# Kernel tuning notes

Hardware: AMD Instinct MI355X
Metric: run time of the kernel (lower is better)

## Reference

```python
import jax, jax.numpy as jnp
import numpy as np

B, LQ, LM, D, H = 2, 2048, 2048, 1024, 16
DH = D // H  # 64

def setup_inputs() -> dict:
    key = jax.random.key(0)
    ks = jax.random.split(key, 11)
    s = 0.02
    return {
        "query": jax.random.normal(ks[0], (B, LQ, D), jnp.float32),
        "memory": jax.random.normal(ks[1], (B, LM, D), jnp.float32),
        "memory_bias": jax.random.normal(ks[2], (B, LM), jnp.float32),
        "Wq": jax.random.normal(ks[3], (D, D), jnp.float32) * s,
        "bq": jnp.zeros((D,), jnp.float32),
        "Wk": jax.random.normal(ks[4], (D, D), jnp.float32) * s,
        "bk": jnp.zeros((D,), jnp.float32),
        "Wv": jax.random.normal(ks[5], (D, D), jnp.float32) * s,
        "bv": jnp.zeros((D,), jnp.float32),
        "Wo": jax.random.normal(ks[6], (D, D), jnp.float32) * s,
        "bo": jnp.zeros((D,), jnp.float32),
    }

def reference(query, memory, memory_bias, Wq, bq, Wk, bk, Wv, bv, Wo, bo):
    # QKV projections, split into heads: [B, L, H, DH]
    q = (query @ Wq + bq).reshape(B, LQ, H, DH)
    k = (memory @ Wk + bk).reshape(B, LM, H, DH)
    v = (memory @ Wv + bv).reshape(B, LM, H, DH)
    q = q * (DH ** -0.5)
    # logits: [B, H, Lq, Lk] (matches torch.einsum('btnh,bfnh->bnft', k, q))
    logits = jnp.einsum("bfnh,btnh->bnft", q, k)
    logits = logits + memory_bias[:, None, None, :]  # bias [B, Lm] -> [B,1,1,Lk]
    weights = jax.nn.softmax(logits, axis=-1)
    # dropout omitted (eval / rate 0 for correctness baseline)
    attn = jnp.einsum("bnft,btnh->bfnh", weights, v).reshape(B, LQ, D)
    return attn @ Wo + bo  # [B, Lq, output_depth]
```

## Files before the change

kernel.cpp:

```cpp
#include <hip/hip_runtime.h>
#include <hip/hip_bf16.h>
#include <math.h>


typedef __bf16 bf16;
typedef __bf16 bf16x4 __attribute__((ext_vector_type(4)));
typedef __bf16 bf16x8 __attribute__((ext_vector_type(8)));
typedef float f32x4 __attribute__((ext_vector_type(4)));

#define MFMA16(a, b, c) __builtin_amdgcn_mfma_f32_16x16x32_bf16((a), (b), (c), 0, 0, 0)

__device__ inline float exp2_hw(float x) {
    float r; asm("v_exp_f32 %0, %1" : "=v"(r) : "v"(x)); return r;
}

__device__ inline void gload_lds16(const bf16* g, bf16* l) {
    __builtin_amdgcn_global_load_lds(
        (const __attribute__((address_space(1))) void*)g,
        (__attribute__((address_space(3))) void*)l, 16, 0, 0);
}

__global__ __launch_bounds__(256) void cvt_kernel(
    const float* __restrict__ X0, const float* __restrict__ X1,
    bf16* __restrict__ Y0, bf16* __restrict__ Y1)
{
    const float* X = blockIdx.y ? X1 : X0;
    bf16* Y = blockIdx.y ? Y1 : Y0;
    const size_t i = ((size_t)blockIdx.x * 256 + threadIdx.x) * 8;
    float4 f0 = *(const float4*)&X[i];
    float4 f1 = *(const float4*)&X[i + 4];
    bf16x8 h;
    h[0] = (bf16)f0.x; h[1] = (bf16)f0.y; h[2] = (bf16)f0.z; h[3] = (bf16)f0.w;
    h[4] = (bf16)f1.x; h[5] = (bf16)f1.y; h[6] = (bf16)f1.z; h[7] = (bf16)f1.w;
    *(bf16x8*)&Y[i] = h;
}

__global__ __launch_bounds__(256) void transpose_cvt_kernel(
    const float* __restrict__ W0, const float* __restrict__ W1,
    const float* __restrict__ W2, const float* __restrict__ W3,
    bf16* __restrict__ T0, bf16* __restrict__ T1,
    bf16* __restrict__ T2, bf16* __restrict__ T3)
{
    __shared__ float Ls[64][65];
    const float* W; bf16* T;
    switch (blockIdx.z) {
        case 0:  W = W0; T = T0; break;
        case 1:  W = W1; T = T1; break;
        case 2:  W = W2; T = T2; break;
        default: W = W3; T = T3; break;
    }
    const int t = threadIdx.x;
    const int n0 = blockIdx.x * 64, k0 = blockIdx.y * 64;
    const int g = t >> 4, c = (t & 15) * 4;

    #pragma unroll
    for (int p = 0; p < 4; ++p) {
        const int row = p * 16 + g;
        float4 f = *(const float4*)&W[(size_t)(k0 + row) * 1024 + n0 + c];
        Ls[row][c + 0] = f.x; Ls[row][c + 1] = f.y;
        Ls[row][c + 2] = f.z; Ls[row][c + 3] = f.w;
    }
    __syncthreads();
    #pragma unroll
    for (int p = 0; p < 4; ++p) {
        const int n = p * 16 + g;
        bf16x4 h;
        h[0] = (bf16)Ls[c + 0][n]; h[1] = (bf16)Ls[c + 1][n];
        h[2] = (bf16)Ls[c + 2][n]; h[3] = (bf16)Ls[c + 3][n];
        *(bf16x4*)&T[(size_t)(n0 + n) * 1024 + k0 + c] = h;
    }
}

template <typename TO>
__global__ __launch_bounds__(256) void gemm_kernel(
    const bf16* __restrict__ A, const bf16* __restrict__ WT,
    const float* __restrict__ bias, TO* __restrict__ out,
    float alpha, int mode)
{
    __shared__ __align__(16) bf16 As[2][128 * 64];
    __shared__ __align__(16) bf16 Bs[2][64 * 64];

    const int fid = blockIdx.x + (blockIdx.y << 4);
    const int swz = (fid & 7) * 64 + (fid >> 3);
    const int n0 = (swz & 15) * 64;
    const int m0 = (swz >> 4) * 128;

    const int tid = threadIdx.x;
    const int w = tid >> 6, lane = tid & 63;
    const int lr = lane & 15, lg = lane >> 4;
    const int wm = (w >> 1) * 64, wn = (w & 1) * 32;

    const int arow0 = w * 32 + (lane >> 3);
    const int brow0 = w * 16 + (lane >> 3);
    const int sch = lane & 7;

    f32x4 acc[4][2] = {};

    auto stageG = [&](int kt, int bi) {
        #pragma unroll
        for (int p = 0; p < 4; ++p) {
            const int row = arow0 + p * 8;
            const int xc = ((sch ^ (row & 7)) << 3);
            gload_lds16(&A[(size_t)(m0 + row) * 1024 + kt + xc],
                        &As[bi][row * 64 + sch * 8]);
        }
        #pragma unroll
        for (int p = 0; p < 2; ++p) {
            const int row = brow0 + p * 8;
            const int xc = ((sch ^ (row & 7)) << 3);
            gload_lds16(&WT[(size_t)(n0 + row) * 1024 + kt + xc],
                        &Bs[bi][row * 64 + sch * 8]);
        }
    };

    stageG(0, 0);
    __syncthreads();

    int cur = 0;
    #pragma unroll 1
    for (int t = 0; t < 16; ++t) {
        if (t < 15) stageG((t + 1) * 64, cur ^ 1);

        #pragma unroll
        for (int ks = 0; ks < 2; ++ks) {
            const int c = (((ks * 4 + lg) ^ (lr & 7)) << 3);
            bf16x8 af[4], bfv[2];
            #pragma unroll
            for (int mt = 0; mt < 4; ++mt)
                af[mt] = *(const bf16x8*)&As[cur][(wm + mt * 16 + lr) * 64 + c];
            #pragma unroll
            for (int nt = 0; nt < 2; ++nt)
                bfv[nt] = *(const bf16x8*)&Bs[cur][(wn + nt * 16 + lr) * 64 + c];
            #pragma unroll
            for (int nt = 0; nt < 2; ++nt)
                #pragma unroll
                for (int mt = 0; mt < 4; ++mt)
                    acc[mt][nt] = MFMA16(af[mt], bfv[nt], acc[mt][nt]);
        }
        __syncthreads();
        cur ^= 1;
    }

    #pragma unroll
    for (int nt = 0; nt < 2; ++nt) {
        const int n = n0 + wn + nt * 16 + lr;
        const float bv = bias[n];
        #pragma unroll
        for (int mt = 0; mt < 4; ++mt) {
            #pragma unroll
            for (int i = 0; i < 4; ++i) {
                const int m = m0 + wm + mt * 16 + lg * 4 + i;
                const float v = (acc[mt][nt][i] + bv) * alpha;
                if (mode == 0) {
                    out[(size_t)m * 1024 + n] = (TO)v;
                } else {
                    const int b = m >> 11, t2 = m & 2047;
                    out[((size_t)(b << 10) + n) * 2048 + t2] = (TO)v;
                }
            }
        }
    }
}

__global__ __launch_bounds__(512, 4) void attn_kernel(
    const bf16* __restrict__ Q, const bf16* __restrict__ K,
    const bf16* __restrict__ Vt, const float* __restrict__ mbias,
    bf16* __restrict__ Oout)
{
    __shared__ __align__(16) bf16 Kbuf[2][4096];
    __shared__ __align__(16) bf16 Vbuf[2][4096];
    __shared__ bf16 Ps[8][16][76];

    const int tid = threadIdx.x;
    const int w = tid >> 6, lane = tid & 63;
    const int lr = lane & 15, lg = lane >> 4;

    const int fid = blockIdx.x + (blockIdx.y << 4) + (blockIdx.z << 8);
    const int swz = (fid & 7) * 64 + (fid >> 3);
    const int qt = swz & 15, h = (swz >> 4) & 15, b = swz >> 8;
    const int qrow = qt * 128 + w * 16;

    const size_t qo = (size_t)(b * 2048 + qrow + lr) * 1024 + h * 64;
    bf16x8 qf[2];
    qf[0] = *(const bf16x8*)&Q[qo + lg * 8];
    qf[1] = *(const bf16x8*)&Q[qo + 32 + lg * 8];

    const bf16* Kb = K + (size_t)b * 2048 * 1024 + h * 64;
    const bf16* Vb = Vt + ((size_t)b * 1024 + h * 64) * 2048;
    const float* bp = mbias + b * 2048 + lr;

    float m_run[4];
    f32x4 of[4] = {};
    f32x4 ofl = {};
    #pragma unroll
    for (int i = 0; i < 4; ++i) m_run[i] = -INFINITY;

    bf16x8 ones8;
    #pragma unroll
    for (int j = 0; j < 8; ++j) ones8[j] = (bf16)1.0f;

    const int chunk = w * 64 + lane;
    const int sR = chunk >> 3, scs = (chunk & 7) ^ (sR & 7);
    auto stage = [&](int t, int bi) {
        gload_lds16(Kb + (size_t)(t * 64 + sR) * 1024 + scs * 8,
                    &Kbuf[bi][chunk * 8]);
        gload_lds16(Vb + (size_t)sR * 2048 + t * 64 + scs * 8,
                    &Vbuf[bi][chunk * 8]);
    };

    stage(0, 0);
    float bvv[4];
    #pragma unroll
    for (int nt = 0; nt < 4; ++nt) bvv[nt] = bp[nt * 16] * 1.44269504f;

    #pragma unroll 1
    for (int it = 0; it < 32; ++it) {
        const int cur = it & 1;
        stage(it < 31 ? it + 1 : 31, cur ^ 1);
        asm volatile("s_waitcnt vmcnt(2)" ::: "memory");
        __builtin_amdgcn_s_barrier();
        __builtin_amdgcn_sched_barrier(0);

        f32x4 s[4];
        #pragma unroll
        for (int nt = 0; nt < 4; ++nt) {
            s[nt][0] = bvv[nt]; s[nt][1] = bvv[nt];
            s[nt][2] = bvv[nt]; s[nt][3] = bvv[nt];
        }
        #pragma unroll
        for (int ks = 0; ks < 2; ++ks) {
            const int cw = (((ks * 4 + lg) ^ (lr & 7)) << 3);
            bf16x8 kf[4];
            #pragma unroll
            for (int nt = 0; nt < 4; ++nt)
                kf[nt] = *(const bf16x8*)&Kbuf[cur][(nt * 16 + lr) * 64 + cw];
            __builtin_amdgcn_s_setprio(1);
            #pragma unroll
            for (int nt = 0; nt < 4; ++nt)
                s[nt] = MFMA16(qf[ks], kf[nt], s[nt]);
            __builtin_amdgcn_s_setprio(0);
        }

        float rml[4];
        #pragma unroll
        for (int i = 0; i < 4; ++i)
            rml[i] = fmaxf(fmaxf(s[0][i], s[1][i]), fmaxf(s[2][i], s[3][i]));
        bool need = false;
        #pragma unroll
        for (int i = 0; i < 4; ++i)
            need = need || (rml[i] > m_run[i] + 8.f);

        if (__any(need)) {
            #pragma unroll
            for (int off = 1; off < 16; off <<= 1)
                #pragma unroll
                for (int i = 0; i < 4; ++i)
                    rml[i] = fmaxf(rml[i], __shfl_xor(rml[i], off, 64));
            #pragma unroll
            for (int i = 0; i < 4; ++i) {
                const float mnew = fmaxf(m_run[i], rml[i]);
                const float al = exp2_hw(m_run[i] - mnew);
                m_run[i] = mnew;
                ofl[i] *= al;
                #pragma unroll
                for (int dt = 0; dt < 4; ++dt) of[dt][i] *= al;
            }
        }

        bp += (it < 31) ? 64 : 0;
        #pragma unroll
        for (int nt = 0; nt < 4; ++nt) bvv[nt] = bp[nt * 16] * 1.44269504f;

        #pragma unroll
        for (int nt = 0; nt < 4; ++nt)
            #pragma unroll
            for (int i = 0; i < 4; ++i) {
                const float p = exp2_hw(s[nt][i] - m_run[i]);
                Ps[w][lg * 4 + i][nt * 16 + lr] = (bf16)p;
            }

        bf16x8 vf[2][4];
        #pragma unroll
        for (int ks = 0; ks < 2; ++ks) {
            const int cw = (((ks * 4 + lg) ^ (lr & 7)) << 3);
            #pragma unroll
            for (int dt = 0; dt < 4; ++dt)
                vf[ks][dt] = *(const bf16x8*)&Vbuf[cur][(dt * 16 + lr) * 64 + cw];
        }
        bf16x8 pa0 = *(const bf16x8*)&Ps[w][lr][lg * 8];
        bf16x8 pa1 = *(const bf16x8*)&Ps[w][lr][32 + lg * 8];
        __builtin_amdgcn_s_setprio(1);
        #pragma unroll
        for (int dt = 0; dt < 4; ++dt) of[dt] = MFMA16(pa0, vf[0][dt], of[dt]);
        ofl = MFMA16(pa0, ones8, ofl);
        #pragma unroll
        for (int dt = 0; dt < 4; ++dt) of[dt] = MFMA16(pa1, vf[1][dt], of[dt]);
        ofl = MFMA16(pa1, ones8, ofl);
        __builtin_amdgcn_s_setprio(0);

        __builtin_amdgcn_sched_barrier(0);
        __builtin_amdgcn_s_barrier();
    }

    const size_t ob = (size_t)(b * 2048 + qrow + lg * 4) * 1024 + h * 64;
    #pragma unroll
    for (int i = 0; i < 4; ++i) {
        const float inv = 1.0f / ofl[i];
        #pragma unroll
        for (int dt = 0; dt < 4; ++dt)
            Oout[ob + (size_t)i * 1024 + dt * 16 + lr] = (bf16)(of[dt][i] * inv);
    }
}

extern "C" void kernel_launch(void* const* d_in, const int* in_sizes, int n_in,
                              void* d_out, int out_size, void* d_ws, size_t ws_size,
                              hipStream_t stream) {
    const float* query  = (const float*)d_in[0];
    const float* memory = (const float*)d_in[1];
    const float* mbias  = (const float*)d_in[2];
    const float* Wq = (const float*)d_in[3];
    const float* bq = (const float*)d_in[4];
    const float* Wk = (const float*)d_in[5];
    const float* bk = (const float*)d_in[6];
    const float* Wv = (const float*)d_in[7];
    const float* bv = (const float*)d_in[8];
    const float* Wo = (const float*)d_in[9];
    const float* bo = (const float*)d_in[10];
    float* out = (float*)d_out;

    const size_t SZ = 4096ull * 1024ull * sizeof(bf16);
    const size_t WZ = 1024ull * 1024ull * sizeof(bf16);
    char* ws = (char*)d_ws;
    bf16* Qp  = (bf16*)(ws);
    bf16* Kp  = (bf16*)(ws + SZ);
    bf16* Vtp = (bf16*)(ws + 2 * SZ);
    bf16* Ap  = (bf16*)(ws + 3 * SZ);
    bf16* WTq = (bf16*)(ws + 4 * SZ);
    bf16* WTk = (bf16*)(ws + 4 * SZ + WZ);
    bf16* WTv = (bf16*)(ws + 4 * SZ + 2 * WZ);
    bf16* WTo = (bf16*)(ws + 4 * SZ + 3 * WZ);

    dim3 blk(256);
    cvt_kernel<<<dim3(2048, 2), blk, 0, stream>>>(query, memory, Kp, Ap);
    transpose_cvt_kernel<<<dim3(16, 16, 4), blk, 0, stream>>>(
        Wq, Wk, Wv, Wo, WTq, WTk, WTv, WTo);

    dim3 gg(16, 32);
    gemm_kernel<bf16><<<gg, blk, 0, stream>>>(Kp, WTq, bq, Qp,  0.18033688f, 0);
    gemm_kernel<bf16><<<gg, blk, 0, stream>>>(Ap, WTk, bk, Kp,  1.0f, 0);
    gemm_kernel<bf16><<<gg, blk, 0, stream>>>(Ap, WTv, bv, Vtp, 1.0f, 1);
    attn_kernel<<<dim3(16, 16, 2), dim3(512), 0, stream>>>(Qp, Kp, Vtp, mbias, Ap);
    gemm_kernel<float><<<gg, blk, 0, stream>>>(Ap, WTo, bo, out, 1.0f, 0);
}
```

Measured before the change: 150.1 us.

## Fuse K/V projections and rework attention into transposed register-resident softmax

Replaces the separate K and V projection GEMMs with one kernel that reads each activation tile once and computes both outputs. The attention kernel computes S transposed (K as the A operand), so P stays in registers as the B operand of the PV MFMA. This removes the shared-memory P staging and the per-row max shuffles. It also deepens the K/V pipeline to four slots with prefetch distance two, permutes K rows to match the register P layout, and vectorizes the bias loads and output stores. The costs are more LDS per block (which may lower occupancy), more registers from the doubled accumulators in the fused GEMM, and a riskier row permutation.

```diff
diff --git a/kernel.cpp b/kernel.cpp
--- a/kernel.cpp
+++ b/kernel.cpp
@@ -162,14 +162,107 @@
     }
 }
 
+__global__ __launch_bounds__(256) void gemm_kv_kernel(
+    const bf16* __restrict__ A, const bf16* __restrict__ WTk,
+    const bf16* __restrict__ WTv, const float* __restrict__ bk,
+    const float* __restrict__ bv, bf16* __restrict__ Kout,
+    bf16* __restrict__ Vtout)
+{
+    __shared__ __align__(16) bf16 As[2][128 * 64];
+    __shared__ __align__(16) bf16 Bk[2][64 * 64];
+    __shared__ __align__(16) bf16 Bv[2][64 * 64];
+
+    const int fid = blockIdx.x + (blockIdx.y << 4);
+    const int swz = (fid & 7) * 64 + (fid >> 3);
+    const int n0 = (swz & 15) * 64;
+    const int m0 = (swz >> 4) * 128;
+
+    const int tid = threadIdx.x;
+    const int w = tid >> 6, lane = tid & 63;
+    const int lr = lane & 15, lg = lane >> 4;
+    const int wm = (w >> 1) * 64, wn = (w & 1) * 32;
+
+    const int arow0 = w * 32 + (lane >> 3);
+    const int brow0 = w * 16 + (lane >> 3);
+    const int sch = lane & 7;
+
+    f32x4 accK[4][2] = {}, accV[4][2] = {};
+
+    auto stageG = [&](int kt, int bi) {
+        #pragma unroll
+        for (int p = 0; p < 4; ++p) {
+            const int row = arow0 + p * 8;
+            const int xc = ((sch ^ (row & 7)) << 3);
+            gload_lds16(&A[(size_t)(m0 + row) * 1024 + kt + xc],
+                        &As[bi][row * 64 + sch * 8]);
+        }
+        #pragma unroll
+        for (int p = 0; p < 2; ++p) {
+            const int row = brow0 + p * 8;
+            const int xc = ((sch ^ (row & 7)) << 3);
+            gload_lds16(&WTk[(size_t)(n0 + row) * 1024 + kt + xc],
+                        &Bk[bi][row * 64 + sch * 8]);
+            gload_lds16(&WTv[(size_t)(n0 + row) * 1024 + kt + xc],
+                        &Bv[bi][row * 64 + sch * 8]);
+        }
+    };
+
+    stageG(0, 0);
+    __syncthreads();
+
+    int cur = 0;
+    #pragma unroll 1
+    for (int t = 0; t < 16; ++t) {
+        if (t < 15) stageG((t + 1) * 64, cur ^ 1);
+
+        #pragma unroll
+        for (int ks = 0; ks < 2; ++ks) {
+            const int c = (((ks * 4 + lg) ^ (lr & 7)) << 3);
+            bf16x8 af[4], bkf[2], bvf[2];
+            #pragma unroll
+            for (int mt = 0; mt < 4; ++mt)
+                af[mt] = *(const bf16x8*)&As[cur][(wm + mt * 16 + lr) * 64 + c];
+            #pragma unroll
+            for (int nt = 0; nt < 2; ++nt) {
+                bkf[nt] = *(const bf16x8*)&Bk[cur][(wn + nt * 16 + lr) * 64 + c];
+                bvf[nt] = *(const bf16x8*)&Bv[cur][(wn + nt * 16 + lr) * 64 + c];
+            }
+            #pragma unroll
+            for (int nt = 0; nt < 2; ++nt)
+                #pragma unroll
+                for (int mt = 0; mt < 4; ++mt) {
+                    accK[mt][nt] = MFMA16(af[mt], bkf[nt], accK[mt][nt]);
+                    accV[mt][nt] = MFMA16(af[mt], bvf[nt], accV[mt][nt]);
+                }
+        }
+        __syncthreads();
+        cur ^= 1;
+    }
+
+    #pragma unroll
+    for (int nt = 0; nt < 2; ++nt) {
+        const int n = n0 + wn + nt * 16 + lr;
+        const float bkv = bk[n], bvv = bv[n];
+        #pragma unroll
+        for (int mt = 0; mt < 4; ++mt) {
+            #pragma unroll
+            for (int i = 0; i < 4; ++i) {
+                const int m = m0 + wm + mt * 16 + lg * 4 + i;
+                Kout[(size_t)m * 1024 + n] = (bf16)(accK[mt][nt][i] + bkv);
+                const int b = m >> 11, t2 = m & 2047;
+                Vtout[((size_t)(b << 10) + n) * 2048 + t2] = (bf16)(accV[mt][nt][i] + bvv);
+            }
+        }
+    }
+}
+
 __global__ __launch_bounds__(512, 4) void attn_kernel(
     const bf16* __restrict__ Q, const bf16* __restrict__ K,
     const bf16* __restrict__ Vt, const float* __restrict__ mbias,
     bf16* __restrict__ Oout)
 {
-    __shared__ __align__(16) bf16 Kbuf[2][4096];
-    __shared__ __align__(16) bf16 Vbuf[2][4096];
-    __shared__ bf16 Ps[8][16][76];
+    __shared__ __align__(16) bf16 Kbuf[4][4096];
+    __shared__ __align__(16) bf16 Vbuf[4][4096];
 
     const int tid = threadIdx.x;
     const int w = tid >> 6, lane = tid & 63;
@@ -177,138 +270,136 @@
 
     const int fid = blockIdx.x + (blockIdx.y << 4) + (blockIdx.z << 8);
     const int swz = (fid & 7) * 64 + (fid >> 3);
-    const int qt = swz & 15, h = (swz >> 4) & 15, b = swz >> 8;
+    const int qt = swz & 15, head = (swz >> 4) & 15, b = swz >> 8;
     const int qrow = qt * 128 + w * 16;
 
-    const size_t qo = (size_t)(b * 2048 + qrow + lr) * 1024 + h * 64;
+    const size_t qo = (size_t)(b * 2048 + qrow + lr) * 1024 + head * 64;
     bf16x8 qf[2];
     qf[0] = *(const bf16x8*)&Q[qo + lg * 8];
     qf[1] = *(const bf16x8*)&Q[qo + 32 + lg * 8];
 
-    const bf16* Kb = K + (size_t)b * 2048 * 1024 + h * 64;
-    const bf16* Vb = Vt + ((size_t)b * 1024 + h * 64) * 2048;
-    const float* bp = mbias + b * 2048 + lr;
-
-    float m_run[4];
+    const bf16* Kb = K + (size_t)b * 2048 * 1024 + head * 64;
+    const bf16* Vb = Vt + ((size_t)b * 1024 + head * 64) * 2048;
+    const float* biasb = mbias + b * 2048;
+
+    float m_run = -INFINITY;
     f32x4 of[4] = {};
     f32x4 ofl = {};
-    #pragma unroll
-    for (int i = 0; i < 4; ++i) m_run[i] = -INFINITY;
 
     bf16x8 ones8;
     #pragma unroll
     for (int j = 0; j < 8; ++j) ones8[j] = (bf16)1.0f;
 
     const int chunk = w * 64 + lane;
-    const int sR = chunk >> 3, scs = (chunk & 7) ^ (sR & 7);
-    auto stage = [&](int t, int bi) {
-        gload_lds16(Kb + (size_t)(t * 64 + sR) * 1024 + scs * 8,
-                    &Kbuf[bi][chunk * 8]);
-        gload_lds16(Vb + (size_t)sR * 2048 + t * 64 + scs * 8,
-                    &Vbuf[bi][chunk * 8]);
+    const int R = chunk >> 3, cc = chunk & 7;
+    const int cs = cc ^ (R & 7);
+    const int piR = ((R & 16) << 1) | ((R & 12) << 1) | ((R & 32) >> 3) | (R & 3);
+    auto stage = [&](int t, int slot) {
+        gload_lds16(Kb + (size_t)(t * 64 + piR) * 1024 + cs * 8,
+                    &Kbuf[slot][chunk * 8]);
+        gload_lds16(Vb + (size_t)R * 2048 + t * 64 + cs * 8,
+                    &Vbuf[slot][chunk * 8]);
     };
 
     stage(0, 0);
-    float bvv[4];
-    #pragma unroll
-    for (int nt = 0; nt < 4; ++nt) bvv[nt] = bp[nt * 16] * 1.44269504f;
+    stage(1, 1);
+
+    const float L2E = 1.44269504f;
+    f32x4 b4[4];
+    b4[0] = *(const f32x4*)&biasb[8 * lg];
+    b4[1] = *(const f32x4*)&biasb[32 + 8 * lg];
+    b4[2] = *(const f32x4*)&biasb[4 + 8 * lg];
+    b4[3] = *(const f32x4*)&biasb[36 + 8 * lg];
+    #pragma unroll
+    for (int nt = 0; nt < 4; ++nt) b4[nt] *= L2E;
 
     #pragma unroll 1
     for (int it = 0; it < 32; ++it) {
-        const int cur = it & 1;
-        stage(it < 31 ? it + 1 : 31, cur ^ 1);
-        asm volatile("s_waitcnt vmcnt(2)" ::: "memory");
+        const int slot = it & 3;
+        const int tn = (it < 30) ? it + 2 : 31;
+        stage(tn, (it + 2) & 3);
+        asm volatile("s_waitcnt vmcnt(4)" ::: "memory");
         __builtin_amdgcn_s_barrier();
         __builtin_amdgcn_sched_barrier(0);
 
         f32x4 s[4];
         #pragma unroll
-        for (int nt = 0; nt < 4; ++nt) {
-            s[nt][0] = bvv[nt]; s[nt][1] = bvv[nt];
-            s[nt][2] = bvv[nt]; s[nt][3] = bvv[nt];
-        }
+        for (int nt = 0; nt < 4; ++nt) s[nt] = b4[nt];
         #pragma unroll
         for (int ks = 0; ks < 2; ++ks) {
             const int cw = (((ks * 4 + lg) ^ (lr & 7)) << 3);
             bf16x8 kf[4];
             #pragma unroll
             for (int nt = 0; nt < 4; ++nt)
-                kf[nt] = *(const bf16x8*)&Kbuf[cur][(nt * 16 + lr) * 64 + cw];
+                kf[nt] = *(const bf16x8*)&Kbuf[slot][(nt * 16 + lr) * 64 + cw];
             __builtin_amdgcn_s_setprio(1);
             #pragma unroll
             for (int nt = 0; nt < 4; ++nt)
-                s[nt] = MFMA16(qf[ks], kf[nt], s[nt]);
+                s[nt] = MFMA16(kf[nt], qf[ks], s[nt]);
             __builtin_amdgcn_s_setprio(0);
         }
 
-        float rml[4];
-        #pragma unroll
-        for (int i = 0; i < 4; ++i)
-            rml[i] = fmaxf(fmaxf(s[0][i], s[1][i]), fmaxf(s[2][i], s[3][i]));
-        bool need = false;
-        #pragma unroll
-        for (int i = 0; i < 4; ++i)
-            need = need || (rml[i] > m_run[i] + 8.f);
-
-        if (__any(need)) {
-            #pragma unroll
-            for (int off = 1; off < 16; off <<= 1)
-                #pragma unroll
-                for (int i = 0; i < 4; ++i)
-                    rml[i] = fmaxf(rml[i], __shfl_xor(rml[i], off, 64));
-            #pragma unroll
-            for (int i = 0; i < 4; ++i) {
-                const float mnew = fmaxf(m_run[i], rml[i]);
-                const float al = exp2_hw(m_run[i] - mnew);
-                m_run[i] = mnew;
-                ofl[i] *= al;
-                #pragma unroll
-                for (int dt = 0; dt < 4; ++dt) of[dt][i] *= al;
-            }
-        }
-
-        bp += (it < 31) ? 64 : 0;
-        #pragma unroll
-        for (int nt = 0; nt < 4; ++nt) bvv[nt] = bp[nt * 16] * 1.44269504f;
-
+        const int bt = (it < 31) ? (it + 1) * 64 : 31 * 64;
+        f32x4 b4n[4];
+        b4n[0] = *(const f32x4*)&biasb[bt + 8 * lg];
+        b4n[1] = *(const f32x4*)&biasb[bt + 32 + 8 * lg];
+        b4n[2] = *(const f32x4*)&biasb[bt + 4 + 8 * lg];
+        b4n[3] = *(const f32x4*)&biasb[bt + 36 + 8 * lg];
+
+        float rml = s[0][0];
         #pragma unroll
         for (int nt = 0; nt < 4; ++nt)
             #pragma unroll
-            for (int i = 0; i < 4; ++i) {
-                const float p = exp2_hw(s[nt][i] - m_run[i]);
-                Ps[w][lg * 4 + i][nt * 16 + lr] = (bf16)p;
-            }
-
-        bf16x8 vf[2][4];
+            for (int i = 0; i < 4; ++i) rml = fmaxf(rml, s[nt][i]);
+
+        if (__any(rml > m_run + 8.f)) {
+            float mx = fmaxf(rml, __shfl_xor(rml, 16, 64));
+            mx = fmaxf(mx, __shfl_xor(mx, 32, 64));
+            const float mnew = fmaxf(m_run, mx);
+            const float al = exp2_hw(m_run - mnew);
+            m_run = mnew;
+            ofl *= al;
+            #pragma unroll
+            for (int dt = 0; dt < 4; ++dt) of[dt] *= al;
+        }
+
+        bf16x8 pb0, pb1;
+        #pragma unroll
+        for (int i = 0; i < 4; ++i) {
+            pb0[i]     = (bf16)exp2_hw(s[0][i] - m_run);
+            pb1[i]     = (bf16)exp2_hw(s[1][i] - m_run);
+            pb0[4 + i] = (bf16)exp2_hw(s[2][i] - m_run);
+            pb1[4 + i] = (bf16)exp2_hw(s[3][i] - m_run);
+        }
+
+        __builtin_amdgcn_s_setprio(1);
         #pragma unroll
         for (int ks = 0; ks < 2; ++ks) {
             const int cw = (((ks * 4 + lg) ^ (lr & 7)) << 3);
+            const bf16x8 pb = ks ? pb1 : pb0;
+            bf16x8 vf[4];
             #pragma unroll
             for (int dt = 0; dt < 4; ++dt)
-                vf[ks][dt] = *(const bf16x8*)&Vbuf[cur][(dt * 16 + lr) * 64 + cw];
-        }
-        bf16x8 pa0 = *(const bf16x8*)&Ps[w][lr][lg * 8];
-        bf16x8 pa1 = *(const bf16x8*)&Ps[w][lr][32 + lg * 8];
-        __builtin_amdgcn_s_setprio(1);
-        #pragma unroll
-        for (int dt = 0; dt < 4; ++dt) of[dt] = MFMA16(pa0, vf[0][dt], of[dt]);
-        ofl = MFMA16(pa0, ones8, ofl);
-        #pragma unroll
-        for (int dt = 0; dt < 4; ++dt) of[dt] = MFMA16(pa1, vf[1][dt], of[dt]);
-        ofl = MFMA16(pa1, ones8, ofl);
+                vf[dt] = *(const bf16x8*)&Vbuf[slot][(dt * 16 + lr) * 64 + cw];
+            #pragma unroll
+            for (int dt = 0; dt < 4; ++dt)
+                of[dt] = MFMA16(vf[dt], pb, of[dt]);
+            ofl = MFMA16(ones8, pb, ofl);
+        }
         __builtin_amdgcn_s_setprio(0);
 
-        __builtin_amdgcn_sched_barrier(0);
-        __builtin_amdgcn_s_barrier();
-    }
-
-    const size_t ob = (size_t)(b * 2048 + qrow + lg * 4) * 1024 + h * 64;
-    #pragma unroll
-    for (int i = 0; i < 4; ++i) {
-        const float inv = 1.0f / ofl[i];
-        #pragma unroll
-        for (int dt = 0; dt < 4; ++dt)
-            Oout[ob + (size_t)i * 1024 + dt * 16 + lr] = (bf16)(of[dt][i] * inv);
+        #pragma unroll
+        for (int nt = 0; nt < 4; ++nt) b4[nt] = b4n[nt] * L2E;
+    }
+
+    const float inv = 1.0f / ofl[0];
+    const size_t ob = (size_t)(b * 2048 + qrow + lr) * 1024 + head * 64;
+    #pragma unroll
+    for (int dt = 0; dt < 4; ++dt) {
+        bf16x4 h4;
+        #pragma unroll
+        for (int i = 0; i < 4; ++i) h4[i] = (bf16)(of[dt][i] * inv);
+        *(bf16x4*)&Oout[ob + dt * 16 + lg * 4] = h4;
     }
 }
 
@@ -346,9 +437,8 @@
         Wq, Wk, Wv, Wo, WTq, WTk, WTv, WTo);
 
     dim3 gg(16, 32);
-    gemm_kernel<bf16><<<gg, blk, 0, stream>>>(Kp, WTq, bq, Qp,  0.18033688f, 0);
-    gemm_kernel<bf16><<<gg, blk, 0, stream>>>(Ap, WTk, bk, Kp,  1.0f, 0);
-    gemm_kernel<bf16><<<gg, blk, 0, stream>>>(Ap, WTv, bv, Vtp, 1.0f, 1);
+    gemm_kernel<bf16><<<gg, blk, 0, stream>>>(Kp, WTq, bq, Qp, 0.18033688f, 0);
+    gemm_kv_kernel<<<gg, blk, 0, stream>>>(Ap, WTk, WTv, bk, bv, Kp, Vtp);
     attn_kernel<<<dim3(16, 16, 2), dim3(512), 0, stream>>>(Qp, Kp, Vtp, mbias, Ap);
     gemm_kernel<float><<<gg, blk, 0, stream>>>(Ap, WTo, bo, out, 1.0f, 0);
 }
```

New measurement: 125.0 us. 1.2x faster.
